# Optimization experiments

Measured on AMD Instinct MI355X. Metric: run time of the kernel, lower is better.

Reference implementation:

```python
import jax, jax.numpy as jnp
import numpy as np

N_Q = 4       # n_qubits
PATCH = 3
PAD = 1       # patch_size // 2


def _u3(theta, phi, lam):
    # U3 gate matrix (2x2 complex)
    c = jnp.cos(theta / 2)
    s = jnp.sin(theta / 2)
    row0 = jnp.stack([c + 0j, -jnp.exp(1j * lam) * s])
    row1 = jnp.stack([jnp.exp(1j * phi) * s, jnp.exp(1j * (phi + lam)) * c])
    return jnp.stack([row0, row1]).astype(jnp.complex64)


def _apply_1q(state, U, wire):
    # state: (N,2,2,2,2) complex; U: (2,2) shared or (N,2,2) batched
    s = jnp.moveaxis(state, 1 + wire, -1)
    shp = s.shape
    s = s.reshape(s.shape[0], -1, 2)
    if U.ndim == 2:
        out = jnp.einsum('ij,nrj->nri', U, s)
    else:
        out = jnp.einsum('nij,nrj->nri', U, s)
    return jnp.moveaxis(out.reshape(shp), -1, 1 + wire)


def _apply_2q(state, U4, cw, tw):
    # U4: (4,4) on (control, target) subspace ordered |c t>
    s = jnp.moveaxis(state, (1 + cw, 1 + tw), (-2, -1))
    shp = s.shape
    s = s.reshape(s.shape[0], -1, 4)
    out = jnp.einsum('ij,nrj->nri', U4, s)
    return jnp.moveaxis(out.reshape(shp), (-2, -1), (1 + cw, 1 + tw))


def setup_inputs() -> dict:
    key = jax.random.key(0)
    ks = jax.random.split(key, 8)
    B, C, H, W = 16, 64, 64, 64
    out_ch = 128
    d_in = C * PATCH * PATCH  # 576
    x = jax.random.normal(ks[0], (B, C, H, W), dtype=jnp.float32)
    fc1_w = jax.random.normal(ks[1], (N_Q, d_in), dtype=jnp.float32) * (1.0 / np.sqrt(d_in))
    fc1_b = jax.random.normal(ks[2], (N_Q,), dtype=jnp.float32) * 0.01
    u3_params = jax.random.normal(ks[3], (N_Q, 3), dtype=jnp.float32)
    cu3_params = jax.random.normal(ks[4], (N_Q, 3), dtype=jnp.float32)
    fc_w = jax.random.normal(ks[5], (out_ch, N_Q), dtype=jnp.float32) * 0.5
    fc_b = jax.random.normal(ks[6], (out_ch,), dtype=jnp.float32) * 0.01
    return {"x": x, "fc1_w": fc1_w, "fc1_b": fc1_b, "u3_params": u3_params,
            "cu3_params": cu3_params, "fc_w": fc_w, "fc_b": fc_b}


def reference(x, fc1_w, fc1_b, u3_params, cu3_params, fc_w, fc_b):
    B, C, H, W = x.shape
    xp = jnp.pad(x, ((0, 0), (0, 0), (PAD, PAD), (PAD, PAD)))
    Hout, Wout = H, W  # stride 1, same padding
    # im2col: feature order (C, di, dj) matches torch patch.reshape(B,-1)
    cols = jnp.stack([xp[:, :, di:di + Hout, dj:dj + Wout]
                      for di in range(PATCH) for dj in range(PATCH)], axis=2)  # (B,C,9,H,W)
    patches = cols.transpose(0, 3, 4, 1, 2).reshape(B, Hout * Wout, C * PATCH * PATCH)
    ang = patches @ fc1_w.T + fc1_b  # (B, P, 4) rotation angles
    Np = B * Hout * Wout
    ang = ang.reshape(Np, N_Q)
    # initial state |0000> for every (batch, patch)
    state = jnp.zeros((Np, 2 ** N_Q), jnp.complex64).at[:, 0].set(1.0)
    state = state.reshape((Np,) + (2,) * N_Q)
    # RY encoding (per-element angles)
    for w in range(N_Q):
        th = ang[:, w] / 2
        c, s = jnp.cos(th), jnp.sin(th)
        Ury = jnp.stack([jnp.stack([c, -s], -1), jnp.stack([s, c], -1)], -2).astype(jnp.complex64)
        state = _apply_1q(state, Ury, w)
    # trainable U3 on every wire
    for w in range(N_Q):
        state = _apply_1q(state, _u3(u3_params[w, 0], u3_params[w, 1], u3_params[w, 2]), w)
    # circular CU3 ring (0,1),(1,2),(2,3),(3,0)
    for w in range(N_Q):
        U = _u3(cu3_params[w, 0], cu3_params[w, 1], cu3_params[w, 2])
        U4 = jnp.eye(4, dtype=jnp.complex64).at[2:, 2:].set(U)
        state = _apply_2q(state, U4, w, (w + 1) % N_Q)
    # <Z> on each wire
    probs = state.real ** 2 + state.imag ** 2  # (Np,2,2,2,2)
    zv = jnp.array([1.0, -1.0], jnp.float32)
    expz = jnp.stack(
        [(probs * zv.reshape((1,) + (1,) * w + (2,) + (1,) * (N_Q - 1 - w))).sum(axis=(1, 2, 3, 4))
         for w in range(N_Q)], axis=1)  # (Np,4)
    out = expz.reshape(B, Hout * Wout, N_Q) @ fc_w.T + fc_b  # (B,P,out_ch)
    out_ch = fc_w.shape[0]
    # faithful to original: view(B, out_ch, side_h, side_w) on contiguous (P,out_ch)
    return out.reshape(B, out_ch, Hout, Wout)
```

## Files before the change

kernel.cpp:

```cpp
#include <hip/hip_runtime.h>
#include <hip/hip_bf16.h>
#include <math.h>

typedef unsigned short u16;
typedef unsigned int   u32;
typedef unsigned long long u64;

#define WS_W2    0
#define WS_B4    2304
#define WS_FCW   2308
#define WS_FCB   2820
#define WS_GATES 2948
#define WS_FLAG  3012
#define WS_PART  4096

__device__ inline float bfbits2f(u32 lo16) {
    u32 u = lo16 << 16;
    return __builtin_bit_cast(float, u);
}
__device__ inline float bchi(u32 w) {
    return __builtin_bit_cast(float, w & 0xffff0000u);
}
__device__ inline float bclo(u32 w) {
    return __builtin_bit_cast(float, w << 16);
}
__device__ inline u16 f2bf(float f) {
    u32 u = __builtin_bit_cast(u32, f);
    u = u + 0x7fffu + ((u >> 16) & 1u);
    return (u16)(u >> 16);
}
__device__ inline float ld_param(const void* p, int i, int isbf16) {
    return isbf16 ? bfbits2f(((const u16*)p)[i]) : ((const float*)p)[i];
}

__global__ __launch_bounds__(256) void k0_prep(
        const void* __restrict__ x,
        const void* __restrict__ fc1_w, const void* __restrict__ fc1_b,
        const void* __restrict__ u3p,   const void* __restrict__ cu3p,
        const void* __restrict__ fc_w,  const void* __restrict__ fc_b,
        float* __restrict__ ws) {
    __shared__ int sflag;
    int t = threadIdx.x;
    if (t == 0) {
        const u32* xw = (const u32*)x;
        int cnt = 0;
        for (int i = 0; i < 64; ++i) {
            u32 e = (xw[i] >> 7) & 0xFFu;
            if (e >= 110 && e <= 130) ++cnt;
        }
        sflag = (cnt >= 32) ? 1 : 0;
        ws[WS_FLAG] = (float)sflag;
    }
    __syncthreads();
    const int bf = sflag;
    u32* wpk = (u32*)ws + WS_W2;
    for (int idx = t; idx < 1152; idx += 256) {
        int c = idx / 18;
        int rem = idx - c * 18;
        int r = rem / 6;
        int p = rem - r * 6;
        int i0 = 2 * p, i1 = 2 * p + 1;
        int q0 = i0 / 3, d0 = i0 - 3 * q0;
        int q1 = i1 / 3, d1 = i1 - 3 * q1;
        u32 lo = f2bf(ld_param(fc1_w, q0 * 576 + c * 9 + r * 3 + d0, bf));
        u32 hi = f2bf(ld_param(fc1_w, q1 * 576 + c * 9 + r * 3 + d1, bf));
        wpk[idx] = lo | (hi << 16);
    }
    if (t < 4)   ws[WS_B4 + t] = ld_param(fc1_b, t, bf);
    for (int idx = t; idx < 512; idx += 256) ws[WS_FCW + idx] = ld_param(fc_w, idx, bf);
    if (t < 128) ws[WS_FCB + t] = ld_param(fc_b, t, bf);
    if (t < 8) {
        int w = t & 3;
        const void* p = (t < 4) ? u3p : cu3p;
        float th = ld_param(p, w * 3 + 0, bf);
        float ph = ld_param(p, w * 3 + 1, bf);
        float la = ld_param(p, w * 3 + 2, bf);
        float c = cosf(0.5f * th), s = sinf(0.5f * th);
        float cl = cosf(la), sl = sinf(la);
        float cp = cosf(ph), sp = sinf(ph);
        float cpl = cp * cl - sp * sl, spl = sp * cl + cp * sl;
        float* m = ws + WS_GATES + t * 8;
        m[0] = c;        m[1] = 0.f;
        m[2] = -cl * s;  m[3] = -sl * s;
        m[4] = cp * s;   m[5] = sp * s;
        m[6] = cpl * c;  m[7] = spl * c;
    }
}

__global__ __launch_bounds__(256) void kA_conv(
        const void* __restrict__ x, const float* __restrict__ ws,
        float4* __restrict__ part) {
    __shared__ u32 tile[24 * 34];
    __shared__ float4 red4[256];
    const int t = threadIdx.x;
    const int bid = blockIdx.x;
    const int cg  = bid & 7;
    const int row = (bid >> 3) & 63;
    const int b   = bid >> 9;
    const int bf = (ws[WS_FLAG] != 0.0f) ? 1 : 0;
    const int c0 = cg * 8;
    const int tc = t >> 6;

    const int cs = __builtin_amdgcn_readfirstlane(c0 + tc * 2);
    const u32* wpk = (const u32*)ws + WS_W2 + cs * 18;
    u32 w36[36];
#pragma unroll
    for (int i = 0; i < 36; ++i) w36[i] = wpk[i];

    const u32*    xu = (const u32*)x;
    const float2* xf = (const float2*)x;
    const int xbase = b * 131072;

    {
        const int jj = t & 31;
        const int g8 = t >> 5;
#pragma unroll
        for (int i = 0; i < 3; ++i) {
            int rowcl = g8 + i * 8;
            int r = rowcl >> 3, cl = rowcl & 7;
            int gr = row - 1 + r;
            u32 pk = 0;
            if (gr >= 0 && gr < 64) {
                int idx = xbase + (c0 + cl) * 2048 + gr * 32 + jj;
                if (bf) pk = xu[idx];
                else { float2 v = xf[idx];
                       pk = (u32)f2bf(v.x) | ((u32)f2bf(v.y) << 16); }
            }
            tile[rowcl * 34 + 1 + jj] = pk;
        }
        if (t < 48) { int rc = t >> 1; tile[rc * 34 + ((t & 1) ? 33 : 0)] = 0u; }
    }
    __syncthreads();

    const int j = t & 63;
    const int pj = (j + 1) >> 1;
    const int sh = (1 - (j & 1)) * 16;
    float ang0 = 0.f, ang1 = 0.f, ang2 = 0.f, ang3 = 0.f;
#pragma unroll
    for (int cc = 0; cc < 2; ++cc) {
        const int cl = tc * 2 + cc;
#pragma unroll
        for (int r = 0; r < 3; ++r) {
            const u32* rp = tile + (r * 8 + cl) * 34 + pj;
            u32 lo = rp[0], hi = rp[1];
            u64 v = (((u64)hi << 32) | lo) >> sh;
            u32 vlo = (u32)v, vhi = (u32)(v >> 32);
            float e0 = bclo(vlo);
            float e1 = bchi(vlo);
            float e2 = bclo(vhi);
            const int wb = cc * 18 + r * 6;
            u32 u0 = w36[wb], u1 = w36[wb + 1], u2 = w36[wb + 2];
            u32 u3 = w36[wb + 3], u4 = w36[wb + 4], u5 = w36[wb + 5];
            ang0 += e0 * bclo(u0) + e1 * bchi(u0) + e2 * bclo(u1);
            ang1 += e0 * bchi(u1) + e1 * bclo(u2) + e2 * bchi(u2);
            ang2 += e0 * bclo(u3) + e1 * bchi(u3) + e2 * bclo(u4);
            ang3 += e0 * bchi(u4) + e1 * bclo(u5) + e2 * bchi(u5);
        }
    }

    red4[tc * 64 + j] = make_float4(ang0, ang1, ang2, ang3);
    __syncthreads();
    if (t < 64) {
        float4 a0 = red4[t], a1 = red4[64 + t], a2 = red4[128 + t], a3 = red4[192 + t];
        float4 s = make_float4(a0.x + a1.x + a2.x + a3.x,
                               a0.y + a1.y + a2.y + a3.y,
                               a0.z + a1.z + a2.z + a3.z,
                               a0.w + a1.w + a2.w + a3.w);
        part[cg * 65536 + b * 4096 + row * 64 + t] = s;
    }
}

__global__ __launch_bounds__(256) void kB_circuit_fc(
        const float* __restrict__ ws, const float4* __restrict__ part,
        void* __restrict__ out) {
    __shared__ float4 smEz[64];
    const int t = threadIdx.x;
    const int bp0 = blockIdx.x * 64;
    const int bf = (ws[WS_FLAG] != 0.0f) ? 1 : 0;

    if (t < 64) {
        const int bp = bp0 + t;
        float ax = 0.f, ay = 0.f, az = 0.f, aw = 0.f;
#pragma unroll
        for (int g = 0; g < 8; ++g) {
            float4 a = part[g * 65536 + bp];
            ax += a.x; ay += a.y; az += a.z; aw += a.w;
        }
        float angf[4];
        angf[0] = ws[WS_B4 + 0] + ax;
        angf[1] = ws[WS_B4 + 1] + ay;
        angf[2] = ws[WS_B4 + 2] + az;
        angf[3] = ws[WS_B4 + 3] + aw;

        const float* G = ws + WS_GATES;
        float vr[4][2], vi[4][2];
#pragma unroll
        for (int w = 0; w < 4; ++w) {
            float sa, ca;
            __sincosf(0.5f * angf[w], &sa, &ca);
            const float* m = G + w * 8;
            vr[w][0] = m[0] * ca + m[2] * sa;  vi[w][0] = m[1] * ca + m[3] * sa;
            vr[w][1] = m[4] * ca + m[6] * sa;  vi[w][1] = m[5] * ca + m[7] * sa;
        }
        float t01r[4], t01i[4], t23r[4], t23i[4];
#pragma unroll
        for (int a = 0; a < 2; ++a)
#pragma unroll
            for (int bq = 0; bq < 2; ++bq) {
                t01r[a * 2 + bq] = vr[0][a] * vr[1][bq] - vi[0][a] * vi[1][bq];
                t01i[a * 2 + bq] = vr[0][a] * vi[1][bq] + vi[0][a] * vr[1][bq];
                t23r[a * 2 + bq] = vr[2][a] * vr[3][bq] - vi[2][a] * vi[3][bq];
                t23i[a * 2 + bq] = vr[2][a] * vi[3][bq] + vi[2][a] * vr[3][bq];
            }
        float ar[16], ai[16];
#pragma unroll
        for (int n = 0; n < 16; ++n) {
            int hi = n >> 2, lo = n & 3;
            ar[n] = t01r[hi] * t23r[lo] - t01i[hi] * t23i[lo];
            ai[n] = t01r[hi] * t23i[lo] + t01i[hi] * t23r[lo];
        }
#pragma unroll
        for (int w = 0; w < 4; ++w) {
            const float* m = G + 32 + w * 8;
            const int cb = 8 >> w;
            const int tb = 8 >> ((w + 1) & 3);
#pragma unroll
            for (int n = 0; n < 16; ++n) {
                if ((n & cb) != 0 && (n & tb) == 0) {
                    int n1 = n | tb;
                    float a0r = ar[n], a0i = ai[n], a1r = ar[n1], a1i = ai[n1];
                    ar[n]  = m[0] * a0r - m[1] * a0i + m[2] * a1r - m[3] * a1i;
                    ai[n]  = m[0] * a0i + m[1] * a0r + m[2] * a1i + m[3] * a1r;
                    ar[n1] = m[4] * a0r - m[5] * a0i + m[6] * a1r - m[7] * a1i;
                    ai[n1] = m[4] * a0i + m[5] * a0r + m[6] * a1i + m[7] * a1r;
                }
            }
        }
        float ez[4] = {0.f, 0.f, 0.f, 0.f};
#pragma unroll
        for (int n = 0; n < 16; ++n) {
            float pr = ar[n] * ar[n] + ai[n] * ai[n];
#pragma unroll
            for (int w = 0; w < 4; ++w)
                ez[w] += ((n >> (3 - w)) & 1) ? -pr : pr;
        }
        smEz[t] = make_float4(ez[0], ez[1], ez[2], ez[3]);
    }
    __syncthreads();

    const int og = (t & 15) * 8;
    const float4* fw4 = (const float4*)(ws + WS_FCW) + og;
    const float*  fbp = ws + WS_FCB + og;
    float4 w0 = fw4[0], w1 = fw4[1], w2 = fw4[2], w3 = fw4[3];
    float4 w4 = fw4[4], w5 = fw4[5], w6 = fw4[6], w7 = fw4[7];
    float4 bA = *(const float4*)fbp, bB = *(const float4*)(fbp + 4);
#pragma unroll
    for (int ch = 0; ch < 4; ++ch) {
        const int pl = (t >> 4) + ch * 16;
        const float4 ez = smEz[pl];
        float v0 = bA.x + ez.x*w0.x + ez.y*w0.y + ez.z*w0.z + ez.w*w0.w;
        float v1 = bA.y + ez.x*w1.x + ez.y*w1.y + ez.z*w1.z + ez.w*w1.w;
        float v2 = bA.z + ez.x*w2.x + ez.y*w2.y + ez.z*w2.z + ez.w*w2.w;
        float v3 = bA.w + ez.x*w3.x + ez.y*w3.y + ez.z*w3.z + ez.w*w3.w;
        float v4 = bB.x + ez.x*w4.x + ez.y*w4.y + ez.z*w4.z + ez.w*w4.w;
        float v5 = bB.y + ez.x*w5.x + ez.y*w5.y + ez.z*w5.z + ez.w*w5.w;
        float v6 = bB.z + ez.x*w6.x + ez.y*w6.y + ez.z*w6.z + ez.w*w6.w;
        float v7 = bB.w + ez.x*w7.x + ez.y*w7.y + ez.z*w7.z + ez.w*w7.w;
        if (bf) {
            u32 p0 = (u32)f2bf(v0) | ((u32)f2bf(v1) << 16);
            u32 p1 = (u32)f2bf(v2) | ((u32)f2bf(v3) << 16);
            u32 p2 = (u32)f2bf(v4) | ((u32)f2bf(v5) << 16);
            u32 p3 = (u32)f2bf(v6) | ((u32)f2bf(v7) << 16);
            ((uint4*)out)[blockIdx.x * 1024 + ch * 256 + t] =
                make_uint4(p0, p1, p2, p3);
        } else {
            float4* o = (float4*)out + (blockIdx.x * 2048 + ch * 512 + 2 * t);
            o[0] = make_float4(v0, v1, v2, v3);
            o[1] = make_float4(v4, v5, v6, v7);
        }
    }
}

extern "C" void kernel_launch(void* const* d_in, const int* in_sizes, int n_in,
                              void* d_out, int out_size, void* d_ws, size_t ws_size,
                              hipStream_t stream) {
    float* ws = (float*)d_ws;
    float4* part = (float4*)(ws + WS_PART);
    k0_prep<<<dim3(1), dim3(256), 0, stream>>>(d_in[0], d_in[1], d_in[2], d_in[3],
                                               d_in[4], d_in[5], d_in[6], ws);
    kA_conv<<<dim3(8192), dim3(256), 0, stream>>>(d_in[0], ws, part);
    kB_circuit_fc<<<dim3(1024), dim3(256), 0, stream>>>(ws, part, d_out);
}
```

Baseline: 108.6 us.

## Fuse conv and circuit/FC kernels into one 1024-thread block per row

Merges the per-channel-group conv kernel and the circuit+FC kernel into one kernel where each 1024-thread block handles all 64 channels of one output row, reducing partial angles in shared memory instead of global memory. This removes the partial-sum round trip through global memory and one kernel launch. In exchange, each block now needs a larger shared tile, each thread holds 72 weight registers, and the circuit stage runs on only 64 of 1024 threads while the rest wait at the barrier, which may hurt occupancy and latency hiding.

```diff
diff --git a/kernel.cpp b/kernel.cpp
--- a/kernel.cpp
+++ b/kernel.cpp
@@ -12,7 +12,6 @@
 #define WS_FCB   2820
 #define WS_GATES 2948
 #define WS_FLAG  3012
-#define WS_PART  4096
 
 __device__ inline float bfbits2f(u32 lo16) {
     u32 u = lo16 << 16;
@@ -87,25 +86,24 @@
     }
 }
 
-__global__ __launch_bounds__(256) void kA_conv(
+__global__ __launch_bounds__(1024, 8) void kF(
         const void* __restrict__ x, const float* __restrict__ ws,
-        float4* __restrict__ part) {
-    __shared__ u32 tile[24 * 34];
-    __shared__ float4 red4[256];
+        void* __restrict__ out) {
+    __shared__ u32 tile[192 * 34];
+    __shared__ float4 smEz[64];
+    float4* red = (float4*)tile;
+
     const int t = threadIdx.x;
     const int bid = blockIdx.x;
-    const int cg  = bid & 7;
-    const int row = (bid >> 3) & 63;
-    const int b   = bid >> 9;
+    const int b = bid >> 6, row = bid & 63;
     const int bf = (ws[WS_FLAG] != 0.0f) ? 1 : 0;
-    const int c0 = cg * 8;
-    const int tc = t >> 6;
-
-    const int cs = __builtin_amdgcn_readfirstlane(c0 + tc * 2);
+    const int tcg = t >> 6, j = t & 63;
+
+    const int cs = __builtin_amdgcn_readfirstlane(tcg * 4);
     const u32* wpk = (const u32*)ws + WS_W2 + cs * 18;
-    u32 w36[36];
-#pragma unroll
-    for (int i = 0; i < 36; ++i) w36[i] = wpk[i];
+    u32 w72[72];
+#pragma unroll
+    for (int i = 0; i < 72; ++i) w72[i] = wpk[i];
 
     const u32*    xu = (const u32*)x;
     const float2* xf = (const float2*)x;
@@ -113,35 +111,34 @@
 
     {
         const int jj = t & 31;
-        const int g8 = t >> 5;
-#pragma unroll
-        for (int i = 0; i < 3; ++i) {
-            int rowcl = g8 + i * 8;
-            int r = rowcl >> 3, cl = rowcl & 7;
+        const int seed = t >> 5;
+#pragma unroll
+        for (int i = 0; i < 6; ++i) {
+            int rc = seed + i * 32;
+            int r = rc >> 6, c = rc & 63;
             int gr = row - 1 + r;
             u32 pk = 0;
             if (gr >= 0 && gr < 64) {
-                int idx = xbase + (c0 + cl) * 2048 + gr * 32 + jj;
+                int idx = xbase + c * 2048 + gr * 32 + jj;
                 if (bf) pk = xu[idx];
                 else { float2 v = xf[idx];
                        pk = (u32)f2bf(v.x) | ((u32)f2bf(v.y) << 16); }
             }
-            tile[rowcl * 34 + 1 + jj] = pk;
-        }
-        if (t < 48) { int rc = t >> 1; tile[rc * 34 + ((t & 1) ? 33 : 0)] = 0u; }
-    }
-    __syncthreads();
-
-    const int j = t & 63;
+            tile[rc * 34 + 1 + jj] = pk;
+        }
+        if (t < 384) { int rc = t >> 1; tile[rc * 34 + ((t & 1) ? 33 : 0)] = 0u; }
+    }
+    __syncthreads();
+
     const int pj = (j + 1) >> 1;
     const int sh = (1 - (j & 1)) * 16;
     float ang0 = 0.f, ang1 = 0.f, ang2 = 0.f, ang3 = 0.f;
 #pragma unroll
-    for (int cc = 0; cc < 2; ++cc) {
-        const int cl = tc * 2 + cc;
+    for (int cc = 0; cc < 4; ++cc) {
+        const int c = tcg * 4 + cc;
 #pragma unroll
         for (int r = 0; r < 3; ++r) {
-            const u32* rp = tile + (r * 8 + cl) * 34 + pj;
+            const u32* rp = tile + (r * 64 + c) * 34 + pj;
             u32 lo = rp[0], hi = rp[1];
             u64 v = (((u64)hi << 32) | lo) >> sh;
             u32 vlo = (u32)v, vhi = (u32)(v >> 32);
@@ -149,8 +146,8 @@
             float e1 = bchi(vlo);
             float e2 = bclo(vhi);
             const int wb = cc * 18 + r * 6;
-            u32 u0 = w36[wb], u1 = w36[wb + 1], u2 = w36[wb + 2];
-            u32 u3 = w36[wb + 3], u4 = w36[wb + 4], u5 = w36[wb + 5];
+            u32 u0 = w72[wb], u1 = w72[wb + 1], u2 = w72[wb + 2];
+            u32 u3 = w72[wb + 3], u4 = w72[wb + 4], u5 = w72[wb + 5];
             ang0 += e0 * bclo(u0) + e1 * bchi(u0) + e2 * bclo(u1);
             ang1 += e0 * bchi(u1) + e1 * bclo(u2) + e2 * bchi(u2);
             ang2 += e0 * bclo(u3) + e1 * bchi(u3) + e2 * bclo(u4);
@@ -158,32 +155,15 @@
         }
     }
 
-    red4[tc * 64 + j] = make_float4(ang0, ang1, ang2, ang3);
-    __syncthreads();
+    __syncthreads();
+    red[tcg * 64 + j] = make_float4(ang0, ang1, ang2, ang3);
+    __syncthreads();
+
     if (t < 64) {
-        float4 a0 = red4[t], a1 = red4[64 + t], a2 = red4[128 + t], a3 = red4[192 + t];
-        float4 s = make_float4(a0.x + a1.x + a2.x + a3.x,
-                               a0.y + a1.y + a2.y + a3.y,
-                               a0.z + a1.z + a2.z + a3.z,
-                               a0.w + a1.w + a2.w + a3.w);
-        part[cg * 65536 + b * 4096 + row * 64 + t] = s;
-    }
-}
-
-__global__ __launch_bounds__(256) void kB_circuit_fc(
-        const float* __restrict__ ws, const float4* __restrict__ part,
-        void* __restrict__ out) {
-    __shared__ float4 smEz[64];
-    const int t = threadIdx.x;
-    const int bp0 = blockIdx.x * 64;
-    const int bf = (ws[WS_FLAG] != 0.0f) ? 1 : 0;
-
-    if (t < 64) {
-        const int bp = bp0 + t;
         float ax = 0.f, ay = 0.f, az = 0.f, aw = 0.f;
 #pragma unroll
-        for (int g = 0; g < 8; ++g) {
-            float4 a = part[g * 65536 + bp];
+        for (int g = 0; g < 16; ++g) {
+            float4 a = red[g * 64 + t];
             ax += a.x; ay += a.y; az += a.z; aw += a.w;
         }
         float angf[4];
@@ -236,47 +216,39 @@
                 }
             }
         }
-        float ez[4] = {0.f, 0.f, 0.f, 0.f};
+        float ez0 = 0.f, ez1 = 0.f, ez2 = 0.f, ez3 = 0.f;
 #pragma unroll
         for (int n = 0; n < 16; ++n) {
             float pr = ar[n] * ar[n] + ai[n] * ai[n];
-#pragma unroll
-            for (int w = 0; w < 4; ++w)
-                ez[w] += ((n >> (3 - w)) & 1) ? -pr : pr;
-        }
-        smEz[t] = make_float4(ez[0], ez[1], ez[2], ez[3]);
-    }
-    __syncthreads();
-
-    const int og = (t & 15) * 8;
-    const float4* fw4 = (const float4*)(ws + WS_FCW) + og;
-    const float*  fbp = ws + WS_FCB + og;
-    float4 w0 = fw4[0], w1 = fw4[1], w2 = fw4[2], w3 = fw4[3];
-    float4 w4 = fw4[4], w5 = fw4[5], w6 = fw4[6], w7 = fw4[7];
-    float4 bA = *(const float4*)fbp, bB = *(const float4*)(fbp + 4);
-#pragma unroll
-    for (int ch = 0; ch < 4; ++ch) {
-        const int pl = (t >> 4) + ch * 16;
-        const float4 ez = smEz[pl];
-        float v0 = bA.x + ez.x*w0.x + ez.y*w0.y + ez.z*w0.z + ez.w*w0.w;
-        float v1 = bA.y + ez.x*w1.x + ez.y*w1.y + ez.z*w1.z + ez.w*w1.w;
-        float v2 = bA.z + ez.x*w2.x + ez.y*w2.y + ez.z*w2.z + ez.w*w2.w;
-        float v3 = bA.w + ez.x*w3.x + ez.y*w3.y + ez.z*w3.z + ez.w*w3.w;
-        float v4 = bB.x + ez.x*w4.x + ez.y*w4.y + ez.z*w4.z + ez.w*w4.w;
-        float v5 = bB.y + ez.x*w5.x + ez.y*w5.y + ez.z*w5.z + ez.w*w5.w;
-        float v6 = bB.z + ez.x*w6.x + ez.y*w6.y + ez.z*w6.z + ez.w*w6.w;
-        float v7 = bB.w + ez.x*w7.x + ez.y*w7.y + ez.z*w7.z + ez.w*w7.w;
+            ez0 += (n & 8) ? -pr : pr;
+            ez1 += (n & 4) ? -pr : pr;
+            ez2 += (n & 2) ? -pr : pr;
+            ez3 += (n & 1) ? -pr : pr;
+        }
+        smEz[t] = make_float4(ez0, ez1, ez2, ez3);
+    }
+    __syncthreads();
+
+    {
+        const float4 ez = smEz[t >> 4];
+        const float4* fw4 = (const float4*)(ws + WS_FCW) + (t & 15) * 8;
+        const float*  fbp = ws + WS_FCB + (t & 15) * 8;
+        float v[8];
+#pragma unroll
+        for (int m = 0; m < 8; ++m) {
+            float4 w = fw4[m];
+            v[m] = fbp[m] + ez.x * w.x + ez.y * w.y + ez.z * w.z + ez.w * w.w;
+        }
         if (bf) {
-            u32 p0 = (u32)f2bf(v0) | ((u32)f2bf(v1) << 16);
-            u32 p1 = (u32)f2bf(v2) | ((u32)f2bf(v3) << 16);
-            u32 p2 = (u32)f2bf(v4) | ((u32)f2bf(v5) << 16);
-            u32 p3 = (u32)f2bf(v6) | ((u32)f2bf(v7) << 16);
-            ((uint4*)out)[blockIdx.x * 1024 + ch * 256 + t] =
-                make_uint4(p0, p1, p2, p3);
+            u32 p0 = (u32)f2bf(v[0]) | ((u32)f2bf(v[1]) << 16);
+            u32 p1 = (u32)f2bf(v[2]) | ((u32)f2bf(v[3]) << 16);
+            u32 p2 = (u32)f2bf(v[4]) | ((u32)f2bf(v[5]) << 16);
+            u32 p3 = (u32)f2bf(v[6]) | ((u32)f2bf(v[7]) << 16);
+            ((uint4*)out)[bid * 1024 + t] = make_uint4(p0, p1, p2, p3);
         } else {
-            float4* o = (float4*)out + (blockIdx.x * 2048 + ch * 512 + 2 * t);
-            o[0] = make_float4(v0, v1, v2, v3);
-            o[1] = make_float4(v4, v5, v6, v7);
+            float4* o = (float4*)out + (bid * 2048 + 2 * t);
+            o[0] = make_float4(v[0], v[1], v[2], v[3]);
+            o[1] = make_float4(v[4], v[5], v[6], v[7]);
         }
     }
 }
@@ -285,9 +257,7 @@
                               void* d_out, int out_size, void* d_ws, size_t ws_size,
                               hipStream_t stream) {
     float* ws = (float*)d_ws;
-    float4* part = (float4*)(ws + WS_PART);
     k0_prep<<<dim3(1), dim3(256), 0, stream>>>(d_in[0], d_in[1], d_in[2], d_in[3],
                                                d_in[4], d_in[5], d_in[6], ws);
-    kA_conv<<<dim3(8192), dim3(256), 0, stream>>>(d_in[0], ws, part);
-    kB_circuit_fc<<<dim3(1024), dim3(256), 0, stream>>>(ws, part, d_out);
-}
+    kF<<<dim3(1024), dim3(1024), 0, stream>>>(d_in[0], ws, d_out);
+}
```

After: 134.6 us. 1.24x slower.
